# Performance work log

Measured on AMD Instinct MI355X. Metric: run time of the kernel, lower is better.

The kernel has to match this reference:

```python
import jax, jax.numpy as jnp
import numpy as np

T_, B_, DIM, NB, D, H_, W_ = 4, 4, 256, 16, 16, 32, 32
VTH_L1_LOW = VTH_L1_HIGH = 0.5
EPS = 1e-5

# ---- surrogate-gradient spike (ATan surrogate, alpha=2.0, spikingjelly default) ----
@jax.custom_vjp
def spike(x):
    return (x >= 0).astype(x.dtype)

def _spk_fwd(x):
    return spike(x), x

def _spk_bwd(x, g):
    a = 2.0
    return (g * (a / 2.0) / (1.0 + (jnp.pi / 2.0 * a * x) ** 2),)

spike.defvjp(_spk_fwd, _spk_bwd)

def lif(x, tau=2.0, vth=1.0):
    # MultiStepLIFNode: v += (x - v)/tau; fire at vth; hard reset (detach_reset)
    def step(v, xt):
        v = v + (xt - v) / tau
        s = spike(v - vth)
        v = v * (1.0 - jax.lax.stop_gradient(s))
        return v, s
    _, s = jax.lax.scan(step, jnp.zeros_like(x[0]), x)
    return s

def haar_mat(n):
    m = np.zeros((n, n), np.float32)
    s = 1.0 / np.sqrt(2.0)
    for i in range(n // 2):
        m[i, 2 * i] = s; m[i, 2 * i + 1] = s          # low-pass rows
        m[n // 2 + i, 2 * i] = s; m[n // 2 + i, 2 * i + 1] = -s  # high-pass rows
    return jnp.asarray(m)

def bn(x, g, b):  # training-mode BatchNorm2d over (N,C,H,W)
    mu = jnp.mean(x, axis=(0, 2, 3), keepdims=True)
    var = jnp.var(x, axis=(0, 2, 3), keepdims=True)
    return g.reshape(1, -1, 1, 1) * (x - mu) * jax.lax.rsqrt(var + EPS) + b.reshape(1, -1, 1, 1)

def conv(x, w, b):
    y = jax.lax.conv_general_dilated(x, w, (1, 1), 'SAME',
                                     dimension_numbers=('NCHW', 'OIHW', 'NCHW'))
    return y + b.reshape(1, -1, 1, 1)

def band_gate(c, vth, tau):
    # coefficient spiking threshold then channel-energy sparsity gate
    c = c * spike(jnp.abs(c) - vth)
    E = jnp.mean(c * c, axis=(-2, -1), keepdims=True)  # per (T,B,C) energy
    return c * (E > tau).astype(c.dtype)

def _forward(x, haar_weight, conv1_w, conv1_b, conv2_w, conv2_b,
             bn_fwd_g, bn_fwd_b, bn_mul_g, bn_mul_b, bn_inv_g, bn_inv_b,
             bn_c1_g, bn_c1_b, bn_c2_g, bn_c2_b):
    T, B, C, H, W = x.shape
    HmW, HmH = haar_mat(W), haar_mat(H)
    Hh, Wh, TB = H // 2, W // 2, T * B
    s = lif(x)
    # ---- level-1 Haar along W ----
    y = jnp.einsum('vw,tbchw->tbchv', HmW, s)
    low, high = y[..., :Wh], y[..., Wh:]
    low = low * spike(jnp.abs(low) - VTH_L1_LOW)
    high = high * spike(jnp.abs(high) - VTH_L1_HIGH)
    l1 = jnp.concatenate([low, high], axis=2)  # (T,B,2C,H,Wh)
    l1 = bn(l1.reshape(TB, 2 * C, H, Wh), bn_fwd_g, bn_fwd_b).reshape(T, B, 2 * C, H, Wh)
    # ---- level-2 Haar along H + per-band sparsity ----
    lo, hi = l1[:, :, :C], l1[:, :, C:]
    zlo = jnp.einsum('vh,tbchw->tbcvw', HmH, lo)
    zhi = jnp.einsum('vh,tbchw->tbcvw', HmH, hi)
    LL = band_gate(zlo[..., :Hh, :], 0.5, 0.01)
    HL = band_gate(zlo[..., Hh:, :], 0.5, 0.02)
    LH = band_gate(zhi[..., :Hh, :], 0.5, 0.02)
    HH = band_gate(zhi[..., Hh:, :], 0.5, 0.05)
    l2 = jnp.concatenate([LL, HL, LH, HH], axis=2)  # (T,B,4C,Hh,Wh)
    l2 = bn(l2.reshape(TB, 4 * C, Hh, Wh), bn_mul_g, bn_mul_b)
    # ---- block-diagonal multiply ----
    h = l2.reshape(TB, NB, 4 * D, Hh, Wh).transpose(0, 3, 4, 1, 2)  # (TB,Hh,Wh,NB,4D)
    parts = [jnp.einsum('thwbd,bdk->thwbk', h[..., i * D:(i + 1) * D], haar_weight)
             for i in range(4)]
    h = jnp.concatenate(parts, axis=-1)
    h = h.reshape(TB, Hh, Wh, 4 * C).transpose(0, 3, 1, 2).reshape(T, B, 4 * C, Hh, Wh)
    # ---- inverse Haar ----
    LLc, HLc, LHc, HHc = h[:, :, :C], h[:, :, C:2 * C], h[:, :, 2 * C:3 * C], h[:, :, 3 * C:]
    lo = jnp.einsum('vh,tbcvw->tbchw', HmH, jnp.concatenate([LLc, HLc], axis=-2))
    hi = jnp.einsum('vh,tbcvw->tbchw', HmH, jnp.concatenate([LHc, HHc], axis=-2))
    rec = jnp.einsum('vw,tbchv->tbchw', HmW, jnp.concatenate([lo, hi], axis=-1))
    rec = bn(rec.reshape(TB, C, H, W), bn_inv_g, bn_inv_b).reshape(T, B, C, H, W)
    # ---- conv residual paths over block channels ----
    xr = s.reshape(TB * NB, D, H, W)
    c1 = bn(conv(xr, conv1_w, conv1_b).reshape(TB, C, H, W), bn_c1_g, bn_c1_b).reshape(T, B, C, H, W)
    c2 = bn(conv(xr, conv2_w, conv2_b).reshape(TB, C, H, W), bn_c2_g, bn_c2_b).reshape(T, B, C, H, W)
    return rec + c1 + c2

def setup_inputs() -> dict:
    key = jax.random.key(0)
    ks = jax.random.split(key, 4)
    return {
        'x': jax.random.normal(ks[0], (T_, B_, DIM, H_, W_), jnp.float32),
        'haar_weight': 0.02 * jax.random.normal(ks[1], (NB, D, D), jnp.float32),
        'conv1_w': 0.1 * jax.random.normal(ks[2], (D, D, 1, 1), jnp.float32),
        'conv1_b': jnp.zeros((D,), jnp.float32),
        'conv2_w': 0.05 * jax.random.normal(ks[3], (D, D, 3, 3), jnp.float32),
        'conv2_b': jnp.zeros((D,), jnp.float32),
        'bn_fwd_g': jnp.ones((2 * DIM,), jnp.float32), 'bn_fwd_b': jnp.zeros((2 * DIM,), jnp.float32),
        'bn_mul_g': jnp.ones((4 * DIM,), jnp.float32), 'bn_mul_b': jnp.zeros((4 * DIM,), jnp.float32),
        'bn_inv_g': jnp.ones((DIM,), jnp.float32), 'bn_inv_b': jnp.zeros((DIM,), jnp.float32),
        'bn_c1_g': jnp.ones((DIM,), jnp.float32), 'bn_c1_b': jnp.zeros((DIM,), jnp.float32),
        'bn_c2_g': jnp.ones((DIM,), jnp.float32), 'bn_c2_b': jnp.zeros((DIM,), jnp.float32),
    }

def reference(x, haar_weight, conv1_w, conv1_b, conv2_w, conv2_b,
              bn_fwd_g, bn_fwd_b, bn_mul_g, bn_mul_b, bn_inv_g, bn_inv_b,
              bn_c1_g, bn_c1_b, bn_c2_g, bn_c2_b):
    return _forward(x, haar_weight, conv1_w, conv1_b, conv2_w, conv2_b,
                    bn_fwd_g, bn_fwd_b, bn_mul_g, bn_mul_b, bn_inv_g, bn_inv_b,
                    bn_c1_g, bn_c1_b, bn_c2_g, bn_c2_b)
```

## Files before the change

kernel.cpp:

```cpp
#include <hip/hip_runtime.h>
#include <hip/hip_bf16.h>

#define T_ 4
#define B_ 4
#define C_ 256
#define H_ 32
#define W_ 32
#define TB_ 16
#define Hh_ 16
#define Wh_ 16
#define INVS2 0.70710678118654752440f
#define EPSBN 1e-5f

#define OFF_HW   0
#define OFF_W1   4096
#define OFF_B1   4352
#define OFF_W2   4368
#define OFF_B2   6672
#define OFF_G1   6688
#define OFF_BE1  7200
#define OFF_G2   7712
#define OFF_BE2  8736
#define OFF_G3   9760
#define OFF_BE3  10016
#define OFF_G4   10272
#define OFF_BE4  10528
#define OFF_G5   10784
#define OFF_BE5  11040
#define W_TOTAL  11296
#define NSUMS    4608
#define P1OFF    4608

struct WPtrs { const void* p[15]; };

typedef __attribute__((ext_vector_type(8))) short short8;
typedef __attribute__((ext_vector_type(4))) float f32x4;

__device__ inline float bf2f(__hip_bfloat16 v) { return __bfloat162float(v); }
__device__ inline float bfu(unsigned short u) { return __uint_as_float((unsigned)u << 16); }

__global__ __launch_bounds__(256) void k_lifprep(const void* __restrict__ x_,
                                                 WPtrs wp,
                                                 __hip_bfloat16* __restrict__ wc,
                                                 float* __restrict__ stats,
                                                 int* __restrict__ flag,
                                                 unsigned char* __restrict__ s,
                                                 signed char* __restrict__ l1) {
    int bid = blockIdx.x;
    int tid = threadIdx.x;

    const unsigned short* xr = (const unsigned short*)x_;
    int cnt = 0;
    for (int i = tid; i < 2048; i += 256) {
        int e = (xr[i] >> 7) & 0xFF;
        if (e >= 134) cnt++;
    }
    for (int o = 1; o < 64; o <<= 1) cnt += __shfl_xor(cnt, o, 64);
    __shared__ int sh[4];
    __shared__ float part[4][4];
    if ((tid & 63) == 0) sh[tid >> 6] = cnt;
    __syncthreads();
    int f = (sh[0] + sh[1] + sh[2] + sh[3] >= 32) ? 1 : 0;

    if (bid >= 2048) {
        int pb = bid - 2048;
        if (pb == 0 && tid == 0) *flag = f;
        const int sizes[15] = {4096, 256, 16, 2304, 16, 512, 512, 1024, 1024,
                               256, 256, 256, 256, 256, 256};
        int i = pb * 256 + tid;
        if (i < W_TOTAL) {
            int seg = 0, off = 0;
            while (i >= off + sizes[seg]) { off += sizes[seg]; seg++; }
            int j = i - off;
            float v = f ? ((const float*)wp.p[seg])[j]
                        : bf2f(((const __hip_bfloat16*)wp.p[seg])[j]);
            wc[i] = __float2bfloat16(v);
        }
        if (i < 3584) stats[1024 + i] = 0.f;
        return;
    }

    int half = bid & 1;
    int c = (bid >> 1) & 255;
    int b = bid >> 9;
    int wp_ = tid & 15;
    int hl = tid >> 4;
    int h = half * 16 + hl;
    const float* xf = (const float*)x_;
    const unsigned int* xb = (const unsigned int*)x_;
    int n = ((b * 256 + c) * 32 + h) * 32 + 2 * wp_;

    float v0 = 0.f, v1 = 0.f;
    float aL = 0.f, qL = 0.f, aH = 0.f, qH = 0.f;
    #pragma unroll
    for (int t = 0; t < T_; ++t) {
        size_t idx = (size_t)t * 1048576 + n;
        float x0, x1;
        if (f) {
            float2 xx = *(const float2*)(xf + idx);
            x0 = xx.x; x1 = xx.y;
        } else {
            unsigned int u = xb[idx >> 1];
            x0 = __uint_as_float(u << 16);
            x1 = __uint_as_float(u & 0xffff0000u);
        }
        v0 += (x0 - v0) * 0.5f;
        v1 += (x1 - v1) * 0.5f;
        float s0 = (v0 >= 1.f) ? 1.f : 0.f;
        float s1 = (v1 >= 1.f) ? 1.f : 0.f;
        v0 *= (1.f - s0);
        v1 *= (1.f - s1);
        int tb = t * 4 + b;
        ((uchar2*)s)[(size_t)(tb * 256 + c) * 512 + h * 16 + wp_] =
            make_uchar2((unsigned char)s0, (unsigned char)s1);
        float cl = s0 + s1, ch = s0 - s1;
        size_t lb = (((size_t)tb * 512 + c) * 32 + h) * 16 + wp_;
        l1[lb] = (signed char)(int)cl;
        l1[lb + (size_t)256 * 512] = (signed char)(int)ch;
        aL += cl; qL += cl * cl; aH += ch; qH += ch * ch;
    }
    for (int o = 1; o < 64; o <<= 1) {
        aL += __shfl_xor(aL, o, 64); qL += __shfl_xor(qL, o, 64);
        aH += __shfl_xor(aH, o, 64); qH += __shfl_xor(qH, o, 64);
    }
    int lane = tid & 63, wv = tid >> 6;
    if (lane == 0) {
        part[wv][0] = aL; part[wv][1] = qL; part[wv][2] = aH; part[wv][3] = qH;
    }
    __syncthreads();
    if (tid < 4) {
        float tot = part[0][tid] + part[1][tid] + part[2][tid] + part[3][tid];
        stats[P1OFF + ((b * 2 + half) * 4 + tid) * 256 + c] = tot;
    }
}

struct SharedU {
    union {
        struct {
            short lo[1025 * 8];
            short hi[1025 * 8];
            unsigned short w2s[2304];
            unsigned short w1s[256];
            unsigned short bs[32];
            float parts[4][4][16];
        } cv;
        struct {
            float lo[512];
            float hi[512];
            float part[4][8];
        } s2;
    };
};

__global__ __launch_bounds__(256) void k_work(const unsigned char* __restrict__ s,
                                              const signed char* __restrict__ l1,
                                              const __hip_bfloat16* __restrict__ wc,
                                              float* __restrict__ stats,
                                              __hip_bfloat16* __restrict__ l2,
                                              __hip_bfloat162* __restrict__ cc) {
    __shared__ SharedU sm;
    int bid = blockIdx.x;
    int tid = threadIdx.x;
    int lane = tid & 63, wv = tid >> 6;

    if (bid < 256) {
        int img = bid;
        const unsigned short* wr = (const unsigned short*)wc;
        for (int i = tid; i < 2304; i += 256) sm.cv.w2s[i] = wr[OFF_W2 + i];
        sm.cv.w1s[tid] = wr[OFF_W1 + tid];
        if (tid < 16) { sm.cv.bs[tid] = wr[OFF_B1 + tid]; sm.cv.bs[16 + tid] = wr[OFF_B2 + tid]; }
        if (tid < 8) {
            ((unsigned int*)sm.cv.lo)[4096 + (tid & 3)] = 0;
            ((unsigned int*)sm.cv.hi)[4096 + (tid & 3)] = 0;
        }
        {
            const unsigned int* sp = (const unsigned int*)(s + (size_t)img * 16384);
            int d2 = tid >> 5;
            int pg = tid & 31;
            unsigned int* dst = (unsigned int*)((d2 < 4) ? sm.cv.lo : sm.cv.hi);
            int dl = d2 & 3;
            #pragma unroll
            for (int p = 0; p < 8; ++p) {
                int base = p * 32 + pg;
                unsigned int u0 = sp[d2 * 512 + base];
                unsigned int u1 = sp[d2 * 512 + 256 + base];
                #pragma unroll
                for (int jj = 0; jj < 4; ++jj) {
                    int j = (jj + pg) & 3;
                    unsigned int b0 = (u0 >> (8 * j)) & 255u;
                    unsigned int b1 = (u1 >> (8 * j)) & 255u;
                    unsigned int val = (b0 ? 0x3F80u : 0u) | ((b1 ? 0x3F80u : 0u) << 16);
                    int pix = p * 128 + pg * 4 + j;
                    dst[pix * 4 + dl] = val;
                }
            }
        }
        __syncthreads();

        int m = lane & 15;
        int g = lane >> 4;
        const int tapA[5] = {0, 2, 4, 6, 8};
        const int tapB[5] = {1, 3, 5, 7, 8};

        short8 afr[5], a1f;
        #pragma unroll
        for (int p = 0; p < 5; ++p) {
            int tap = (g < 2) ? tapA[p] : tapB[p];
            short8 av;
            #pragma unroll
            for (int j = 0; j < 8; ++j) {
                int d = (g & 1) * 8 + j;
                unsigned short w = sm.cv.w2s[m * 144 + d * 9 + tap];
                if (p == 4 && g >= 2) w = 0;
                av[j] = (short)w;
            }
            afr[p] = av;
        }
        #pragma unroll
        for (int j = 0; j < 8; ++j) {
            int d = (g & 1) * 8 + j;
            a1f[j] = (g < 2) ? (short)sm.cv.w1s[m * 16 + d] : (short)0;
        }
        float bias1[4], bias2[4];
        #pragma unroll
        for (int r = 0; r < 4; ++r) {
            bias1[r] = bfu(sm.cv.bs[g * 4 + r]);
            bias2[r] = bfu(sm.cv.bs[16 + g * 4 + r]);
        }

        __hip_bfloat162* occ = cc + (size_t)img * 16384;
        const short* bsrc = (g & 1) ? sm.cv.hi : sm.cv.lo;

        float cs1[4] = {0, 0, 0, 0}, cq1[4] = {0, 0, 0, 0};
        float cs2[4] = {0, 0, 0, 0}, cq2[4] = {0, 0, 0, 0};

        for (int t = wv * 16; t < wv * 16 + 16; ++t) {
            int h = t >> 1;
            int w0 = (t & 1) << 4;
            f32x4 acc2 = {0.f, 0.f, 0.f, 0.f};
            f32x4 acc1 = {0.f, 0.f, 0.f, 0.f};
            #pragma unroll
            for (int p = 0; p < 5; ++p) {
                int tap = (g < 2) ? tapA[p] : tapB[p];
                int row = h + tap / 3 - 1;
                int col = w0 + m + (tap % 3) - 1;
                bool ok = ((unsigned)row < 32u) && ((unsigned)col < 32u);
                int idx = ok ? (row * 32 + col) : 1024;
                short8 bv = *(const short8*)&bsrc[idx * 8];
                acc2 = __builtin_amdgcn_mfma_f32_16x16x32_bf16(afr[p], bv, acc2, 0, 0, 0);
                if (p == 2)
                    acc1 = __builtin_amdgcn_mfma_f32_16x16x32_bf16(a1f, bv, acc1, 0, 0, 0);
            }
            int pix = h * 32 + w0 + m;
            #pragma unroll
            for (int r = 0; r < 4; ++r) {
                int k = g * 4 + r;
                float y1 = acc1[r] + bias1[r];
                float y2 = acc2[r] + bias2[r];
                __hip_bfloat162 pr;
                pr.x = __float2bfloat16(y1);
                pr.y = __float2bfloat16(y2);
                occ[(size_t)k * 1024 + pix] = pr;
                cs1[r] += y1; cq1[r] += y1 * y1;
                cs2[r] += y2; cq2[r] += y2 * y2;
            }
        }
        #pragma unroll
        for (int o = 1; o < 16; o <<= 1) {
            #pragma unroll
            for (int r = 0; r < 4; ++r) {
                cs1[r] += __shfl_xor(cs1[r], o, 64);
                cq1[r] += __shfl_xor(cq1[r], o, 64);
                cs2[r] += __shfl_xor(cs2[r], o, 64);
                cq2[r] += __shfl_xor(cq2[r], o, 64);
            }
        }
        if (m == 0) {
            #pragma unroll
            for (int r = 0; r < 4; ++r) {
                sm.cv.parts[wv][g][r * 4 + 0] = cs1[r];
                sm.cv.parts[wv][g][r * 4 + 1] = cq1[r];
                sm.cv.parts[wv][g][r * 4 + 2] = cs2[r];
                sm.cv.parts[wv][g][r * 4 + 3] = cq2[r];
            }
        }
        __syncthreads();
        if (tid < 64) {
            int gg = tid >> 4, r = (tid >> 2) & 3, which = tid & 3;
            float tot = sm.cv.parts[0][gg][r * 4 + which] + sm.cv.parts[1][gg][r * 4 + which]
                      + sm.cv.parts[2][gg][r * 4 + which] + sm.cv.parts[3][gg][r * 4 + which];
            int ch = (img & 15) * 16 + gg * 4 + r;
            const int base[4] = {3584, 3840, 4096, 4352};
            atomicAdd(&stats[base[which] + ch], tot);
        }
    } else {
        int blk = bid - 256;
        int c = blk & 255;
        int tb = blk >> 8;

        const float* p1 = stats + P1OFF;
        float aLs = 0.f, qLs = 0.f, aHs = 0.f, qHs = 0.f;
        #pragma unroll
        for (int slot = 0; slot < 8; ++slot) {
            aLs += p1[(slot * 4 + 0) * 256 + c];
            qLs += p1[(slot * 4 + 1) * 256 + c];
            aHs += p1[(slot * 4 + 2) * 256 + c];
            qHs += p1[(slot * 4 + 3) * 256 + c];
        }

        const float nrm = 1.f / 8192.f;
        float mL = aLs * INVS2 * nrm;
        float vL = fmaxf(qLs * 0.5f * nrm - mL * mL, 0.f);
        float sL = bf2f(wc[OFF_G1 + c]) * rsqrtf(vL + EPSBN);
        float tL = bf2f(wc[OFF_BE1 + c]) - mL * sL;
        float mH = aHs * INVS2 * nrm;
        float vH = fmaxf(qHs * 0.5f * nrm - mH * mH, 0.f);
        float sH = bf2f(wc[OFF_G1 + 256 + c]) * rsqrtf(vH + EPSBN);
        float tH = bf2f(wc[OFF_BE1 + 256 + c]) - mH * sH;

        const signed char* plo = l1 + (((size_t)tb * 512) + c) * (H_ * Wh_);
        const signed char* phi = l1 + (((size_t)tb * 512) + 256 + c) * (H_ * Wh_);
        float slo = sL * INVS2, shi = sH * INVS2;
        {
            int t2 = tid & 127;
            bool isLo = tid < 128;
            int v = isLo ? ((const int*)plo)[t2] : ((const int*)phi)[t2];
            float sc = isLo ? slo : shi;
            float tc = isLo ? tL : tH;
            float* dst = isLo ? sm.s2.lo : sm.s2.hi;
            f32x4 fv;
            #pragma unroll
            for (int j = 0; j < 4; ++j)
                fv[j] = (float)(signed char)((v >> (8 * j)) & 0xFF) * sc + tc;
            *(f32x4*)&dst[t2 * 4] = fv;
        }
        __syncthreads();

        int w = tid & 15, v = tid >> 4;
        float a = sm.s2.lo[(2 * v) * Wh_ + w], b = sm.s2.lo[(2 * v + 1) * Wh_ + w];
        float zLL = (a + b) * INVS2;
        float zHL = (a - b) * INVS2;
        a = sm.s2.hi[(2 * v) * Wh_ + w]; b = sm.s2.hi[(2 * v + 1) * Wh_ + w];
        float zLH = (a + b) * INVS2;
        float zHH = (a - b) * INVS2;
        zLL = (fabsf(zLL) - 0.5f >= 0.f) ? zLL : 0.f;
        zHL = (fabsf(zHL) - 0.5f >= 0.f) ? zHL : 0.f;
        zLH = (fabsf(zLH) - 0.5f >= 0.f) ? zLH : 0.f;
        zHH = (fabsf(zHH) - 0.5f >= 0.f) ? zHH : 0.f;

        float r0 = zLL, r1 = zHL, r2 = zLH, r3 = zHH;
        float q0 = zLL * zLL, q1 = zHL * zHL, q2 = zLH * zLH, q3 = zHH * zHH;
        for (int o = 1; o < 64; o <<= 1) {
            r0 += __shfl_xor(r0, o, 64); r1 += __shfl_xor(r1, o, 64);
            r2 += __shfl_xor(r2, o, 64); r3 += __shfl_xor(r3, o, 64);
            q0 += __shfl_xor(q0, o, 64); q1 += __shfl_xor(q1, o, 64);
            q2 += __shfl_xor(q2, o, 64); q3 += __shfl_xor(q3, o, 64);
        }
        if (lane == 0) {
            sm.s2.part[wv][0] = r0; sm.s2.part[wv][1] = r1;
            sm.s2.part[wv][2] = r2; sm.s2.part[wv][3] = r3;
            sm.s2.part[wv][4] = q0; sm.s2.part[wv][5] = q1;
            sm.s2.part[wv][6] = q2; sm.s2.part[wv][7] = q3;
        }
        __syncthreads();
        float S0 = sm.s2.part[0][0] + sm.s2.part[1][0] + sm.s2.part[2][0] + sm.s2.part[3][0];
        float S1 = sm.s2.part[0][1] + sm.s2.part[1][1] + sm.s2.part[2][1] + sm.s2.part[3][1];
        float S2 = sm.s2.part[0][2] + sm.s2.part[1][2] + sm.s2.part[2][2] + sm.s2.part[3][2];
        float S3 = sm.s2.part[0][3] + sm.s2.part[1][3] + sm.s2.part[2][3] + sm.s2.part[3][3];
        float Q0 = sm.s2.part[0][4] + sm.s2.part[1][4] + sm.s2.part[2][4] + sm.s2.part[3][4];
        float Q1 = sm.s2.part[0][5] + sm.s2.part[1][5] + sm.s2.part[2][5] + sm.s2.part[3][5];
        float Q2 = sm.s2.part[0][6] + sm.s2.part[1][6] + sm.s2.part[2][6] + sm.s2.part[3][6];
        float Q3 = sm.s2.part[0][7] + sm.s2.part[1][7] + sm.s2.part[2][7] + sm.s2.part[3][7];
        float fLL = (Q0 * (1.f / 256.f) > 0.01f) ? 1.f : 0.f;
        float fHL = (Q1 * (1.f / 256.f) > 0.02f) ? 1.f : 0.f;
        float fLH = (Q2 * (1.f / 256.f) > 0.02f) ? 1.f : 0.f;
        float fHH = (Q3 * (1.f / 256.f) > 0.05f) ? 1.f : 0.f;

        float* sums2 = stats + 1024;
        if (tid < 8) {
            const int cho[8] = {0, 1024, 256, 1280, 512, 1536, 768, 1792};
            const float vals[8] = {fLL * S0, fLL * Q0, fHL * S1, fHL * Q1,
                                   fLH * S2, fLH * Q2, fHH * S3, fHH * Q3};
            atomicAdd(&sums2[cho[tid] + c], vals[tid]);
        }

        size_t ob = (((size_t)tb * 1024) + c) * 256 + tid;
        l2[ob]               = __float2bfloat16(zLL * fLL);
        l2[ob + 256u * 256u] = __float2bfloat16(zHL * fHL);
        l2[ob + 512u * 256u] = __float2bfloat16(zLH * fLH);
        l2[ob + 768u * 256u] = __float2bfloat16(zHH * fHH);
    }
}

__global__ __launch_bounds__(256) void k_mixinv(const __hip_bfloat16* __restrict__ l2,
                                                const __hip_bfloat16* __restrict__ wc,
                                                float* __restrict__ stats,
                                                __hip_bfloat16* __restrict__ rec) {
    int bid = blockIdx.x;
    int ks = bid & 3;
    int cg = (bid >> 2) & 15;
    int tb = bid >> 6;
    int tid = threadIdx.x;
    int lane = tid & 63, wvv = tid >> 6;
    const float* sums2 = stats + 1024;

    __shared__ float wt[4][16][4];
    __shared__ float bsc[64], bsh[64];
    __shared__ float parts2[4][8];
    {
        int i = tid;
        int q = i >> 6, rem = i & 63, d = rem >> 2, kk = rem & 3;
        int nb = q * 4 + (cg >> 2);
        int k = ks * 4 + kk;
        wt[q][d][kk] = bf2f(wc[OFF_HW + nb * 256 + d * 16 + k]);
    }
    if (tid < 64) {
        int q = tid >> 4, d = tid & 15;
        int ch = q * 256 + cg * 16 + d;
        float m = sums2[ch] * (1.f / 4096.f);
        float var = fmaxf(sums2[1024 + ch] * (1.f / 4096.f) - m * m, 0.f);
        float sc = bf2f(wc[OFF_G2 + ch]) * rsqrtf(var + EPSBN);
        bsc[tid] = sc;
        bsh[tid] = bf2f(wc[OFF_BE2 + ch]) - m * sc;
    }
    __syncthreads();

    float h[4][4];
    #pragma unroll
    for (int q = 0; q < 4; ++q)
        #pragma unroll
        for (int kk = 0; kk < 4; ++kk) h[q][kk] = 0.f;

    int p = tid;
    #pragma unroll
    for (int q = 0; q < 4; ++q) {
        const __hip_bfloat16* base =
            l2 + ((size_t)tb * 1024 + q * 256 + cg * 16) * 256 + p;
        #pragma unroll
        for (int d = 0; d < 16; ++d) {
            float xv = bf2f(base[d * 256]) * bsc[q * 16 + d] + bsh[q * 16 + d];
            #pragma unroll
            for (int kk = 0; kk < 4; ++kk)
                h[q][kk] = fmaf(xv, wt[q][d][kk], h[q][kk]);
        }
    }

    int uh = tid >> 4, uw = tid & 15;
    __hip_bfloat16* ob = rec + ((size_t)tb * 256 + cg * 16) * 1024;
    float sk[4], qk[4];
    #pragma unroll
    for (int kk = 0; kk < 4; ++kk) {
        int k = ks * 4 + kk;
        float LL = h[0][kk], HL = h[1][kk], LH = h[2][kk], HH = h[3][kk];
        float v00 = 0.5f * (LL + HL + LH + HH);
        float v01 = 0.5f * (LL + HL - LH - HH);
        float v10 = 0.5f * (LL - HL + LH - HH);
        float v11 = 0.5f * (LL - HL - LH + HH);
        __hip_bfloat162 top, bot;
        top.x = __float2bfloat16(v00); top.y = __float2bfloat16(v01);
        bot.x = __float2bfloat16(v10); bot.y = __float2bfloat16(v11);
        *(__hip_bfloat162*)(ob + (size_t)k * 1024 + (2 * uh) * 32 + 2 * uw) = top;
        *(__hip_bfloat162*)(ob + (size_t)k * 1024 + (2 * uh + 1) * 32 + 2 * uw) = bot;
        sk[kk] = v00 + v01 + v10 + v11;
        qk[kk] = v00 * v00 + v01 * v01 + v10 * v10 + v11 * v11;
    }
    for (int o = 1; o < 64; o <<= 1) {
        #pragma unroll
        for (int kk = 0; kk < 4; ++kk) {
            sk[kk] += __shfl_xor(sk[kk], o, 64);
            qk[kk] += __shfl_xor(qk[kk], o, 64);
        }
    }
    if (lane == 0) {
        #pragma unroll
        for (int kk = 0; kk < 4; ++kk) {
            parts2[wvv][kk * 2]     = sk[kk];
            parts2[wvv][kk * 2 + 1] = qk[kk];
        }
    }
    __syncthreads();
    if (tid < 8) {
        int kk = tid >> 1, which = tid & 1;
        float tot = parts2[0][tid] + parts2[1][tid] + parts2[2][tid] + parts2[3][tid];
        atomicAdd(&stats[3072 + which * 256 + cg * 16 + ks * 4 + kk], tot);
    }
}

__global__ __launch_bounds__(256) void k_final(const __hip_bfloat16* __restrict__ rec,
                                               const __hip_bfloat162* __restrict__ cc,
                                               const float* __restrict__ stats,
                                               const __hip_bfloat16* __restrict__ wc,
                                               const int* __restrict__ flag,
                                               void* __restrict__ out_) {
    int n2 = blockIdx.x * 256 + threadIdx.x;
    int c = ((n2 * 2) >> 10) & 255;
    const float inv = 1.f / 16384.f;
    float m3 = stats[3072 + c] * inv;
    float v3 = fmaxf(stats[3328 + c] * inv - m3 * m3, 0.f);
    float sc3 = bf2f(wc[OFF_G3 + c]) * rsqrtf(v3 + EPSBN);
    float sh3 = bf2f(wc[OFF_BE3 + c]) - m3 * sc3;
    float m4 = stats[3584 + c] * inv;
    float v4 = fmaxf(stats[3840 + c] * inv - m4 * m4, 0.f);
    float sc4 = bf2f(wc[OFF_G4 + c]) * rsqrtf(v4 + EPSBN);
    float sh4 = bf2f(wc[OFF_BE4 + c]) - m4 * sc4;
    float m5 = stats[4096 + c] * inv;
    float v5 = fmaxf(stats[4352 + c] * inv - m5 * m5, 0.f);
    float sc5 = bf2f(wc[OFF_G5 + c]) * rsqrtf(v5 + EPSBN);
    float sh5 = bf2f(wc[OFF_BE5 + c]) - m5 * sc5;

    __hip_bfloat162 r = ((const __hip_bfloat162*)rec)[n2];
    __hip_bfloat162 pa = cc[2 * n2];
    __hip_bfloat162 pb = cc[2 * n2 + 1];
    float v0 = bf2f(r.x) * sc3 + sh3 + bf2f(pa.x) * sc4 + sh4 + bf2f(pa.y) * sc5 + sh5;
    float v1 = bf2f(r.y) * sc3 + sh3 + bf2f(pb.x) * sc4 + sh4 + bf2f(pb.y) * sc5 + sh5;
    if (*flag) {
        ((float2*)out_)[n2] = make_float2(v0, v1);
    } else {
        __hip_bfloat162 o;
        o.x = __float2bfloat16(v0); o.y = __float2bfloat16(v1);
        ((__hip_bfloat162*)out_)[n2] = o;
    }
}

extern "C" void kernel_launch(void* const* d_in, const int* in_sizes, int n_in,
                              void* d_out, int out_size, void* d_ws, size_t ws_size,
                              hipStream_t stream) {
    char* ws = (char*)d_ws;
    unsigned char* s_u8  = (unsigned char*)ws;
    signed char* l1c     = (signed char*)(ws + ((size_t)4 << 20));
    __hip_bfloat16* l2   = (__hip_bfloat16*)(ws + ((size_t)8 << 20));
    __hip_bfloat16* rec  = (__hip_bfloat16*)(ws + ((size_t)16 << 20));
    __hip_bfloat162* cc  = (__hip_bfloat162*)(ws + ((size_t)24 << 20));
    __hip_bfloat16* wc   = (__hip_bfloat16*)(ws + ((size_t)40 << 20));
    float* stats         = (float*)(ws + ((size_t)40 << 20) + (64 << 10));
    int* flag            = (int*)(ws + ((size_t)40 << 20) + (128 << 10));

    WPtrs wp;
    for (int i = 0; i < 15; ++i) wp.p[i] = d_in[i + 1];

    dim3 blk(256);
    k_lifprep<<<dim3(2093), blk, 0, stream>>>(d_in[0], wp, wc, stats, flag, s_u8, l1c);
    k_work<<<dim3(4352), blk, 0, stream>>>(s_u8, l1c, wc, stats, l2, cc);
    k_mixinv<<<dim3(1024), blk, 0, stream>>>(l2, wc, stats, rec);
    k_final<<<dim3(8192), blk, 0, stream>>>(rec, cc, stats, wc, flag, d_out);
}
```

Before: 143.1 us.

## Widen LIF loads per thread and interleave level-2 subbands for vector access

```diff
diff --git a/kernel.cpp b/kernel.cpp
--- a/kernel.cpp
+++ b/kernel.cpp
@@ -34,10 +34,16 @@
 struct WPtrs { const void* p[15]; };
 
 typedef __attribute__((ext_vector_type(8))) short short8;
+typedef __attribute__((ext_vector_type(4))) short s16x4;
 typedef __attribute__((ext_vector_type(4))) float f32x4;
 
 __device__ inline float bf2f(__hip_bfloat16 v) { return __bfloat162float(v); }
 __device__ inline float bfu(unsigned short u) { return __uint_as_float((unsigned)u << 16); }
+__device__ inline unsigned short f2bfu(float v) {
+    union { __hip_bfloat16 h; unsigned short u; } c;
+    c.h = __float2bfloat16(v);
+    return c.u;
+}
 
 __global__ __launch_bounds__(256) void k_lifprep(const void* __restrict__ x_,
                                                  WPtrs wp,
@@ -62,8 +68,8 @@
     __syncthreads();
     int f = (sh[0] + sh[1] + sh[2] + sh[3] >= 32) ? 1 : 0;
 
-    if (bid >= 2048) {
-        int pb = bid - 2048;
+    if (bid >= 1024) {
+        int pb = bid - 1024;
         if (pb == 0 && tid == 0) *flag = f;
         const int sizes[15] = {4096, 256, 16, 2304, 16, 512, 512, 1024, 1024,
                                256, 256, 256, 256, 256, 256};
@@ -80,44 +86,56 @@
         return;
     }
 
-    int half = bid & 1;
-    int c = (bid >> 1) & 255;
-    int b = bid >> 9;
-    int wp_ = tid & 15;
-    int hl = tid >> 4;
-    int h = half * 16 + hl;
+    int c = bid & 255;
+    int b = bid >> 8;
+    int wq = tid & 7;
+    int h = tid >> 3;
     const float* xf = (const float*)x_;
-    const unsigned int* xb = (const unsigned int*)x_;
-    int n = ((b * 256 + c) * 32 + h) * 32 + 2 * wp_;
-
-    float v0 = 0.f, v1 = 0.f;
+    int n = ((b * 256 + c) * 32 + h) * 32 + 4 * wq;
+
+    float v0 = 0.f, v1 = 0.f, v2 = 0.f, v3 = 0.f;
     float aL = 0.f, qL = 0.f, aH = 0.f, qH = 0.f;
     #pragma unroll
     for (int t = 0; t < T_; ++t) {
         size_t idx = (size_t)t * 1048576 + n;
-        float x0, x1;
+        float x0, x1, x2, x3;
         if (f) {
-            float2 xx = *(const float2*)(xf + idx);
-            x0 = xx.x; x1 = xx.y;
+            float4 xx = *(const float4*)(xf + idx);
+            x0 = xx.x; x1 = xx.y; x2 = xx.z; x3 = xx.w;
         } else {
-            unsigned int u = xb[idx >> 1];
-            x0 = __uint_as_float(u << 16);
-            x1 = __uint_as_float(u & 0xffff0000u);
+            uint2 u = *(const uint2*)((const char*)x_ + idx * 2);
+            x0 = __uint_as_float(u.x << 16);
+            x1 = __uint_as_float(u.x & 0xffff0000u);
+            x2 = __uint_as_float(u.y << 16);
+            x3 = __uint_as_float(u.y & 0xffff0000u);
         }
         v0 += (x0 - v0) * 0.5f;
         v1 += (x1 - v1) * 0.5f;
+        v2 += (x2 - v2) * 0.5f;
+        v3 += (x3 - v3) * 0.5f;
         float s0 = (v0 >= 1.f) ? 1.f : 0.f;
         float s1 = (v1 >= 1.f) ? 1.f : 0.f;
+        float s2 = (v2 >= 1.f) ? 1.f : 0.f;
+        float s3 = (v3 >= 1.f) ? 1.f : 0.f;
         v0 *= (1.f - s0);
         v1 *= (1.f - s1);
+        v2 *= (1.f - s2);
+        v3 *= (1.f - s3);
         int tb = t * 4 + b;
-        ((uchar2*)s)[(size_t)(tb * 256 + c) * 512 + h * 16 + wp_] =
-            make_uchar2((unsigned char)s0, (unsigned char)s1);
-        float cl = s0 + s1, ch = s0 - s1;
-        size_t lb = (((size_t)tb * 512 + c) * 32 + h) * 16 + wp_;
-        l1[lb] = (signed char)(int)cl;
-        l1[lb + (size_t)256 * 512] = (signed char)(int)ch;
-        aL += cl; qL += cl * cl; aH += ch; qH += ch * ch;
+        *(uchar4*)(s + (size_t)(tb * 256 + c) * 1024 + h * 32 + wq * 4) =
+            make_uchar4((unsigned char)s0, (unsigned char)s1,
+                        (unsigned char)s2, (unsigned char)s3);
+        float cl0 = s0 + s1, ch0 = s0 - s1;
+        float cl1 = s2 + s3, ch1 = s2 - s3;
+        size_t lb = (((size_t)tb * 512 + c) * 32 + h) * 16 + 2 * wq;
+        unsigned short plo = (unsigned short)((unsigned char)(signed char)(int)cl0 |
+                                              ((unsigned char)(signed char)(int)cl1 << 8));
+        unsigned short phi = (unsigned short)((unsigned char)(signed char)(int)ch0 |
+                                              ((unsigned char)(signed char)(int)ch1 << 8));
+        *(unsigned short*)(l1 + lb) = plo;
+        *(unsigned short*)(l1 + lb + (size_t)256 * 512) = phi;
+        aL += cl0 + cl1; qL += cl0 * cl0 + cl1 * cl1;
+        aH += ch0 + ch1; qH += ch0 * ch0 + ch1 * ch1;
     }
     for (int o = 1; o < 64; o <<= 1) {
         aL += __shfl_xor(aL, o, 64); qL += __shfl_xor(qL, o, 64);
@@ -130,7 +148,7 @@
     __syncthreads();
     if (tid < 4) {
         float tot = part[0][tid] + part[1][tid] + part[2][tid] + part[3][tid];
-        stats[P1OFF + ((b * 2 + half) * 4 + tid) * 256 + c] = tot;
+        stats[P1OFF + (b * 4 + tid) * 256 + c] = tot;
     }
 }
 
@@ -301,7 +319,7 @@
         const float* p1 = stats + P1OFF;
         float aLs = 0.f, qLs = 0.f, aHs = 0.f, qHs = 0.f;
         #pragma unroll
-        for (int slot = 0; slot < 8; ++slot) {
+        for (int slot = 0; slot < 4; ++slot) {
             aLs += p1[(slot * 4 + 0) * 256 + c];
             qLs += p1[(slot * 4 + 1) * 256 + c];
             aHs += p1[(slot * 4 + 2) * 256 + c];
@@ -384,11 +402,13 @@
             atomicAdd(&sums2[cho[tid] + c], vals[tid]);
         }
 
-        size_t ob = (((size_t)tb * 1024) + c) * 256 + tid;
-        l2[ob]               = __float2bfloat16(zLL * fLL);
-        l2[ob + 256u * 256u] = __float2bfloat16(zHL * fHL);
-        l2[ob + 512u * 256u] = __float2bfloat16(zLH * fLH);
-        l2[ob + 768u * 256u] = __float2bfloat16(zHH * fHH);
+        size_t ob = (((size_t)tb * 256) + c) * 256 + tid;
+        s16x4 pk;
+        pk[0] = (short)f2bfu(zLL * fLL);
+        pk[1] = (short)f2bfu(zHL * fHL);
+        pk[2] = (short)f2bfu(zLH * fLH);
+        pk[3] = (short)f2bfu(zHH * fHH);
+        *(s16x4*)(l2 + 4 * ob) = pk;
     }
 }
 
@@ -433,12 +453,11 @@
 
     int p = tid;
     #pragma unroll
-    for (int q = 0; q < 4; ++q) {
-        const __hip_bfloat16* base =
-            l2 + ((size_t)tb * 1024 + q * 256 + cg * 16) * 256 + p;
-        #pragma unroll
-        for (int d = 0; d < 16; ++d) {
-            float xv = bf2f(base[d * 256]) * bsc[q * 16 + d] + bsh[q * 16 + d];
+    for (int d = 0; d < 16; ++d) {
+        s16x4 pk = *(const s16x4*)(l2 + 4 * (((size_t)tb * 256 + cg * 16 + d) * 256 + p));
+        #pragma unroll
+        for (int q = 0; q < 4; ++q) {
+            float xv = bfu((unsigned short)pk[q]) * bsc[q * 16 + d] + bsh[q * 16 + d];
             #pragma unroll
             for (int kk = 0; kk < 4; ++kk)
                 h[q][kk] = fmaf(xv, wt[q][d][kk], h[q][kk]);
@@ -539,7 +558,7 @@
     for (int i = 0; i < 15; ++i) wp.p[i] = d_in[i + 1];
 
     dim3 blk(256);
-    k_lifprep<<<dim3(2093), blk, 0, stream>>>(d_in[0], wp, wc, stats, flag, s_u8, l1c);
+    k_lifprep<<<dim3(1069), blk, 0, stream>>>(d_in[0], wp, wc, stats, flag, s_u8, l1c);
     k_work<<<dim3(4352), blk, 0, stream>>>(s_u8, l1c, wc, stats, l2, cc);
     k_mixinv<<<dim3(1024), blk, 0, stream>>>(l2, wc, stats, rec);
     k_final<<<dim3(8192), blk, 0, stream>>>(rec, cc, stats, wc, flag, d_out);
```

New measurement: 139.1 us. 2.8% less time.
